# Kernel optimization log

Measured on AMD Instinct MI355X. Metric: run time of the kernel, lower is better.

The kernel has to match this reference:

```python
import jax, jax.numpy as jnp
import numpy as np

DIM = 128
HOP = 2
NEIGH = [12, 2]  # neighbor_num per hop
ALPHA = 0.2      # leaky-relu slope
NUM_NODE = 50000
B, S = 128, 50
STDV = 1.0 / np.sqrt(DIM)


def _leaky(x):
    return jnp.where(x >= 0, x, ALPHA * x)


def _local_agg(h, adj, a_local):
    # h: [B,S,D], adj: [B,S,S] ints in 0..4, a_local: [4,D]
    a_in = h[:, :, None, :] * h[:, None, :, :]            # [B,S,S,D]
    e = _leaky(jnp.einsum('bijd,kd->kbij', a_in, a_local))  # [4,B,S,S]
    att = jnp.full(adj.shape, -9e15, dtype=h.dtype)
    for k in range(4):
        att = jnp.where(adj == k + 1, e[k], att)
    att = jax.nn.softmax(att, axis=-1)
    return jnp.einsum('bij,bjd->bid', att, h)


def _global_agg(self_v, neigh_v, extra_v, w1, w2, w3, bias):
    # self_v: [B,N,D], neigh_v: [B,N,K,D], extra_v: [B,N,D]
    a = _leaky(jnp.einsum('bnkd,de->bnke', extra_v[:, :, None, :] * neigh_v, w1))
    a = jnp.einsum('bnke,e->bnk', a, w2)
    a = jax.nn.softmax(a, axis=-1)
    agg = jnp.einsum('bnk,bnkd->bnd', a, neigh_v)
    out = jnp.concatenate([self_v, agg], axis=-1) @ w3 + bias
    return jax.nn.relu(out)


def setup_inputs() -> dict:
    key = jax.random.key(0)
    ks = jax.random.split(key, 12)
    u = lambda k, shp: jax.random.uniform(k, shp, jnp.float32, -STDV, STDV)
    return {
        'inputs': jax.random.randint(ks[0], (B, S), 0, NUM_NODE),
        'adj': jax.random.randint(ks[1], (B, S, S), 0, 5),
        'mask_item': jnp.ones((B, S), dtype=jnp.int32),
        'item': jax.random.randint(ks[2], (B, S), 0, NUM_NODE),
        'first_adj': jax.random.randint(ks[3], (B, S * NEIGH[0]), 0, NUM_NODE),
        'adj_all': jax.random.randint(ks[4], (NUM_NODE, 2), 0, NUM_NODE),
        'embedding': u(ks[5], (NUM_NODE, DIM)),
        'a_local': u(ks[6], (4, DIM)),
        'gw1': u(ks[7], (HOP, DIM, DIM)),
        'gw2': u(ks[8], (HOP, DIM)),
        'gw3': u(ks[9], (HOP, 2 * DIM, DIM)),
        'gbias': u(ks[10], (HOP, DIM)),
    }


def reference(inputs, adj, mask_item, item, first_adj, adj_all,
              embedding, a_local, gw1, gw2, gw3, gbias):
    b, s = inputs.shape
    h = embedding[inputs]                                  # [B,S,D]
    h_local = _local_agg(h, adj, a_local)

    m = mask_item.astype(embedding.dtype)[..., None]       # [B,S,1]
    item_emb = embedding[item] * m
    sum_item = jnp.sum(item_emb, 1) / jnp.sum(m, 1)        # [B,D]
    sess = sum_item[:, None, :]                            # [B,1,D]

    # multi-hop neighbor sampling
    neigh1 = first_adj.reshape(b, s * NEIGH[0])            # [B, 600]
    neigh2 = adj_all[neigh1.reshape(-1)].reshape(b, s * NEIGH[0] * NEIGH[1])  # [B,1200]
    ev = [embedding[inputs], embedding[neigh1], embedding[neigh2]]

    for n_hop in range(HOP):
        nxt = []
        for hop in range(HOP - n_hop):
            neigh_v = ev[hop + 1].reshape(b, -1, NEIGH[hop], DIM)
            extra_v = jnp.broadcast_to(sess, (b, ev[hop].shape[1], DIM))
            nxt.append(_global_agg(ev[hop], neigh_v, extra_v,
                                   gw1[n_hop], gw2[n_hop], gw3[n_hop], gbias[n_hop]))
        ev = nxt
    h_global = ev[0].reshape(b, s, DIM)

    # dropout is identity at eval
    return h_local + h_global
```

## Files before the change

kernel.cpp:

```cpp
#include <hip/hip_runtime.h>
#include <stdint.h>

typedef unsigned short ushort_t;
typedef __attribute__((ext_vector_type(8))) short bf16x8;
typedef __attribute__((ext_vector_type(4))) float f32x4;

#define B_   128
#define S_   50
#define D_   128
#define ALPHA_ 0.2f

__device__ __forceinline__ float bf2f(ushort_t u){
  return __uint_as_float(((uint32_t)u) << 16);
}
__device__ __forceinline__ ushort_t f2bf(float f){
  uint32_t x = __float_as_uint(f);
  x = (x + 0x7fffu + ((x >> 16) & 1u)) >> 16;
  return (ushort_t)x;
}
__device__ __forceinline__ float leaky(float x){ return x >= 0.f ? x : ALPHA_*x; }

__global__ void detect_kernel(const uint32_t* __restrict__ emb_raw, int* __restrict__ flag){
  if (threadIdx.x == 0 && blockIdx.x == 0){
    int ok = 1;
    for (int i = 0; i < 64; i++){
      uint32_t lo = emb_raw[i] & 0xffffu;
      uint32_t ex = (lo >> 7) & 0xFFu;
      if (!(lo == 0u || (ex >= 64u && ex <= 126u))) ok = 0;
    }
    *flag = ok;
  }
}

__global__ void cvt_all(const void* __restrict__ p0, const void* __restrict__ p1,
                        const void* __restrict__ p2, const void* __restrict__ p3,
                        const void* __restrict__ p4, const void* __restrict__ p5,
                        ushort_t* __restrict__ dst, const int* __restrict__ flag){
  const int seg_end[6] = {6400000, 6400512, 6433280, 6433536, 6499072, 6499328};
  int base = (blockIdx.x*256 + threadIdx.x) * 4;
  if (base >= 6499328) return;
  int s = 0;
  while (base >= seg_end[s]) s++;
  int segbase = (s == 0) ? 0 : seg_end[s-1];
  const void* src = (s==0)?p0:(s==1)?p1:(s==2)?p2:(s==3)?p3:(s==4)?p4:p5;
  int off = base - segbase;
  union { ushort_t u[4]; uint2 d2; } o;
  if (*flag){
    o.d2 = *(const uint2*)((const ushort_t*)src + off);
  } else {
    float4 v = *(const float4*)((const float*)src + off);
    o.u[0] = f2bf(v.x); o.u[1] = f2bf(v.y); o.u[2] = f2bf(v.z); o.u[3] = f2bf(v.w);
  }
  *(uint2*)(dst + base) = o.d2;
}

__global__ void sess_kernel(const int* __restrict__ item, const int* __restrict__ mask,
                            const ushort_t* __restrict__ emb, ushort_t* __restrict__ sessb){
  int b = blockIdx.x, d = threadIdx.x;
  float acc = 0.f, den = 0.f;
  for (int s = 0; s < S_; s++){
    float fm = (float)mask[b*S_ + s];
    int id = item[b*S_ + s];
    acc += fm * bf2f(emb[(size_t)id*D_ + d]);
    den += fm;
  }
  sessb[b*D_ + d] = f2bf(acc / den);
}

__global__ __launch_bounds__(256) void local_mfma(
    const int* __restrict__ inputs, const int* __restrict__ adj,
    const ushort_t* __restrict__ emb, const ushort_t* __restrict__ alocb,
    ushort_t* __restrict__ hlb){
  __shared__ ushort_t hS[64][136];
  __shared__ ushort_t hT[128][72];
  __shared__ float    attS[64][68];
  __shared__ int      sids[64];
  int b = blockIdx.x;
  int tid = threadIdx.x;
  if (tid < 64) sids[tid] = (tid < S_) ? inputs[b*S_ + tid] : 0;
  __syncthreads();
  for (int idx = tid; idx < 64*128; idx += 256){
    int j = idx >> 7, d = idx & 127;
    ushort_t v = 0;
    if (j < S_) v = emb[(size_t)sids[j]*D_ + d];
    hS[j][d] = v;
    hT[d][j] = v;
  }
  for (int idx = tid; idx < 64*64; idx += 256)
    attS[idx >> 6][idx & 63] = -9.0e15f;
  __syncthreads();

  int lane = tid & 63, wv = tid >> 6;
  int q = lane >> 4, c = lane & 15;

  f32x4 Eacc[4][4];
  #pragma unroll
  for (int mi = 0; mi < 4; mi++)
    #pragma unroll
    for (int ni = 0; ni < 4; ni++) Eacc[mi][ni] = (f32x4){0.f,0.f,0.f,0.f};
  #pragma unroll
  for (int kt = 0; kt < 4; kt++){
    uint4 av = *(const uint4*)(alocb + wv*D_ + kt*32 + q*8);
    const uint32_t* ap = (const uint32_t*)&av;
    union { ushort_t u[8]; bf16x8 v; } afr[4];
    #pragma unroll
    for (int mi = 0; mi < 4; mi++){
      uint4 hv = *(const uint4*)(&hS[mi*16 + c][kt*32 + q*8]);
      const uint32_t* hp = (const uint32_t*)&hv;
      #pragma unroll
      for (int p = 0; p < 4; p++){
        float x0 = __uint_as_float(hp[p] << 16)         * __uint_as_float(ap[p] << 16);
        float x1 = __uint_as_float(hp[p] & 0xffff0000u) * __uint_as_float(ap[p] & 0xffff0000u);
        afr[mi].u[2*p]   = f2bf(x0);
        afr[mi].u[2*p+1] = f2bf(x1);
      }
    }
    #pragma unroll
    for (int ni = 0; ni < 4; ni++){
      union { uint4 q4; bf16x8 v; } bfr;
      bfr.q4 = *(const uint4*)(&hS[ni*16 + c][kt*32 + q*8]);
      #pragma unroll
      for (int mi = 0; mi < 4; mi++)
        Eacc[mi][ni] = __builtin_amdgcn_mfma_f32_16x16x32_bf16(afr[mi].v, bfr.v, Eacc[mi][ni], 0,0,0);
    }
  }
  const int* adjb = adj + (size_t)b*S_*S_;
  #pragma unroll
  for (int mi = 0; mi < 4; mi++){
    #pragma unroll
    for (int ni = 0; ni < 4; ni++){
      int j = ni*16 + c;
      #pragma unroll
      for (int r = 0; r < 4; r++){
        int i = mi*16 + q*4 + r;
        if (i < S_ && j < S_){
          int kk = adjb[i*S_ + j];
          if (kk == wv + 1) attS[i][j] = leaky(Eacc[mi][ni][r]);
        }
      }
    }
  }
  __syncthreads();
  if (tid < 64){
    int i = tid;
    if (i < S_){
      float mx = -__builtin_inff();
      for (int j = 0; j < S_; j++) mx = fmaxf(mx, attS[i][j]);
      float s = 0.f;
      for (int j = 0; j < S_; j++){ float e = __expf(attS[i][j] - mx); attS[i][j] = e; s += e; }
      float inv = 1.f / s;
      for (int j = 0; j < S_; j++) attS[i][j] *= inv;
      for (int j = S_; j < 64; j++) attS[i][j] = 0.f;
    } else {
      for (int j = 0; j < 64; j++) attS[i][j] = 0.f;
    }
  }
  __syncthreads();
  f32x4 Pacc[4][2];
  #pragma unroll
  for (int mi = 0; mi < 4; mi++){ Pacc[mi][0] = (f32x4){0.f,0.f,0.f,0.f}; Pacc[mi][1] = (f32x4){0.f,0.f,0.f,0.f}; }
  #pragma unroll
  for (int kt = 0; kt < 2; kt++){
    union { ushort_t u[8]; bf16x8 v; } afr[4];
    #pragma unroll
    for (int mi = 0; mi < 4; mi++){
      const float* arow = &attS[mi*16 + c][kt*32 + q*8];
      #pragma unroll
      for (int j = 0; j < 8; j++) afr[mi].u[j] = f2bf(arow[j]);
    }
    #pragma unroll
    for (int nn = 0; nn < 2; nn++){
      int ni = 2*wv + nn;
      union { uint4 q4; bf16x8 v; } bfr;
      bfr.q4 = *(const uint4*)(&hT[ni*16 + c][kt*32 + q*8]);
      #pragma unroll
      for (int mi = 0; mi < 4; mi++)
        Pacc[mi][nn] = __builtin_amdgcn_mfma_f32_16x16x32_bf16(afr[mi].v, bfr.v, Pacc[mi][nn], 0,0,0);
    }
  }
  #pragma unroll
  for (int mi = 0; mi < 4; mi++){
    #pragma unroll
    for (int nn = 0; nn < 2; nn++){
      int d = (2*wv + nn)*16 + c;
      #pragma unroll
      for (int r = 0; r < 4; r++){
        int i = mi*16 + q*4 + r;
        if (i < S_) hlb[((size_t)b*S_ + i)*D_ + d] = f2bf(Pacc[mi][nn][r]);
      }
    }
  }
}

__global__ __launch_bounds__(256) void score_mfma_ab(
    const ushort_t* __restrict__ sessb, const ushort_t* __restrict__ emb,
    const int* __restrict__ neigh1, const int* __restrict__ adj_all,
    const ushort_t* __restrict__ w1, const ushort_t* __restrict__ w2,
    float* __restrict__ score, int nA){
  __shared__ uint4 bfrag[2048];
  int tid = threadIdx.x;
  for (int idx = tid; idx < 2048; idx += 256){
    int kt = idx >> 9, rem = idx & 511, t = rem >> 6, ln = rem & 63;
    int qq = ln >> 4, cc = ln & 15;
    union { ushort_t u[8]; uint4 q4; } e;
    #pragma unroll
    for (int j = 0; j < 8; j++)
      e.u[j] = w1[(32*kt + qq*8 + j)*128 + 16*t + cc];
    bfrag[idx] = e.q4;
  }
  __syncthreads();
  int lane = tid & 63, wave = tid >> 6;
  int m = lane & 15, q = lane >> 4;
  float w2v[8];
  #pragma unroll
  for (int t = 0; t < 8; t++) w2v[t] = bf2f(w2[16*t + m]);

  for (int it = 0; it < 2; it++){
    int row_base = blockIdx.x*128 + it*64 + wave*16;
    int row = row_base + m;
    const ushort_t* nrow; int b;
    if (row < nA){
      nrow = emb + (size_t)neigh1[row]*D_;
      b = row / 600;
    } else {
      int r2 = row - nA;
      nrow = emb + (size_t)adj_all[(size_t)neigh1[r2>>1]*2 + (r2&1)]*D_;
      b = r2 / 1200;
    }
    const ushort_t* srow = sessb + (size_t)b*D_;

    f32x4 acc[8];
    #pragma unroll
    for (int t = 0; t < 8; t++) acc[t] = (f32x4){0.f,0.f,0.f,0.f};
    #pragma unroll
    for (int kt = 0; kt < 4; kt++){
      uint4 nv = *(const uint4*)(nrow + kt*32 + q*8);
      uint4 sv = *(const uint4*)(srow + kt*32 + q*8);
      const uint32_t* np = (const uint32_t*)&nv;
      const uint32_t* sp = (const uint32_t*)&sv;
      union { ushort_t u[8]; bf16x8 v; } afr;
      #pragma unroll
      for (int p = 0; p < 4; p++){
        uint32_t n2 = np[p], s2 = sp[p];
        float a0 = __uint_as_float(n2 << 16)          * __uint_as_float(s2 << 16);
        float a1 = __uint_as_float(n2 & 0xffff0000u)  * __uint_as_float(s2 & 0xffff0000u);
        afr.u[2*p]   = f2bf(a0);
        afr.u[2*p+1] = f2bf(a1);
      }
      #pragma unroll
      for (int t = 0; t < 8; t++){
        union { uint4 q4; bf16x8 v; } bfr;
        bfr.q4 = bfrag[(kt*8 + t)*64 + lane];
        acc[t] = __builtin_amdgcn_mfma_f32_16x16x32_bf16(afr.v, bfr.v, acc[t], 0, 0, 0);
      }
    }
    #pragma unroll
    for (int r = 0; r < 4; r++){
      float s = 0.f;
      #pragma unroll
      for (int t = 0; t < 8; t++) s += leaky(acc[t][r]) * w2v[t];
      s += __shfl_xor(s, 1, 64);
      s += __shfl_xor(s, 2, 64);
      s += __shfl_xor(s, 4, 64);
      s += __shfl_xor(s, 8, 64);
      if (m == 0) score[row_base + q*4 + r] = s;
    }
  }
}

__global__ __launch_bounds__(256) void score_mfma_c(
    const ushort_t* __restrict__ sessb, const ushort_t* __restrict__ out1,
    const ushort_t* __restrict__ w1, const ushort_t* __restrict__ w2,
    float* __restrict__ score){
  __shared__ uint4 bfrag[2048];
  int tid = threadIdx.x;
  for (int idx = tid; idx < 2048; idx += 256){
    int kt = idx >> 9, rem = idx & 511, t = rem >> 6, ln = rem & 63;
    int qq = ln >> 4, cc = ln & 15;
    union { ushort_t u[8]; uint4 q4; } e;
    #pragma unroll
    for (int j = 0; j < 8; j++)
      e.u[j] = w1[(32*kt + qq*8 + j)*128 + 16*t + cc];
    bfrag[idx] = e.q4;
  }
  __syncthreads();
  int lane = tid & 63, wave = tid >> 6;
  int m = lane & 15, q = lane >> 4;
  float w2v[8];
  #pragma unroll
  for (int t = 0; t < 8; t++) w2v[t] = bf2f(w2[16*t + m]);
  for (int it = 0; it < 2; it++){
    int row_base = blockIdx.x*128 + it*64 + wave*16;
    int row = row_base + m;
    const ushort_t* nrow = out1 + (size_t)row*D_;
    int b = row / 600;
    const ushort_t* srow = sessb + (size_t)b*D_;
    f32x4 acc[8];
    #pragma unroll
    for (int t = 0; t < 8; t++) acc[t] = (f32x4){0.f,0.f,0.f,0.f};
    #pragma unroll
    for (int kt = 0; kt < 4; kt++){
      uint4 nv = *(const uint4*)(nrow + kt*32 + q*8);
      uint4 sv = *(const uint4*)(srow + kt*32 + q*8);
      const uint32_t* np = (const uint32_t*)&nv;
      const uint32_t* sp = (const uint32_t*)&sv;
      union { ushort_t u[8]; bf16x8 v; } afr;
      #pragma unroll
      for (int p = 0; p < 4; p++){
        uint32_t n2 = np[p], s2 = sp[p];
        float a0 = __uint_as_float(n2 << 16)          * __uint_as_float(s2 << 16);
        float a1 = __uint_as_float(n2 & 0xffff0000u)  * __uint_as_float(s2 & 0xffff0000u);
        afr.u[2*p]   = f2bf(a0);
        afr.u[2*p+1] = f2bf(a1);
      }
      #pragma unroll
      for (int t = 0; t < 8; t++){
        union { uint4 q4; bf16x8 v; } bfr;
        bfr.q4 = bfrag[(kt*8 + t)*64 + lane];
        acc[t] = __builtin_amdgcn_mfma_f32_16x16x32_bf16(afr.v, bfr.v, acc[t], 0, 0, 0);
      }
    }
    #pragma unroll
    for (int r = 0; r < 4; r++){
      float s = 0.f;
      #pragma unroll
      for (int t = 0; t < 8; t++) s += leaky(acc[t][r]) * w2v[t];
      s += __shfl_xor(s, 1, 64);
      s += __shfl_xor(s, 2, 64);
      s += __shfl_xor(s, 4, 64);
      s += __shfl_xor(s, 8, 64);
      if (m == 0) score[row_base + q*4 + r] = s;
    }
  }
}

template<int K>
__device__ __forceinline__ void softmaxK(const float* __restrict__ sc, float att[K]){
  float mx = -__builtin_inff();
  #pragma unroll
  for (int k = 0; k < K; k++){ att[k] = sc[k]; mx = fmaxf(mx, att[k]); }
  float s = 0.f;
  #pragma unroll
  for (int k = 0; k < K; k++){ att[k] = __expf(att[k] - mx); s += att[k]; }
  float inv = 1.f / s;
  #pragma unroll
  for (int k = 0; k < K; k++) att[k] *= inv;
}

template<int K>
__device__ __forceinline__ void out_tile(
    int lane, const uint4* __restrict__ afrag,
    const ushort_t* __restrict__ sptr, const ushort_t* const nptr[K],
    const float att[K], f32x4 acc[8]){
  int q = lane >> 4;
  #pragma unroll
  for (int kt = 0; kt < 8; kt++){
    union { ushort_t u[8]; uint4 q4; bf16x8 v; } bfr;
    if (kt < 4){
      bfr.q4 = *(const uint4*)(sptr + kt*32 + q*8);
    } else {
      float g[8] = {0,0,0,0,0,0,0,0};
      #pragma unroll
      for (int k = 0; k < K; k++){
        uint4 nv = *(const uint4*)(nptr[k] + (kt-4)*32 + q*8);
        const uint32_t* np = (const uint32_t*)&nv;
        #pragma unroll
        for (int p = 0; p < 4; p++){
          g[2*p]   = fmaf(att[k], __uint_as_float(np[p] << 16),         g[2*p]);
          g[2*p+1] = fmaf(att[k], __uint_as_float(np[p] & 0xffff0000u), g[2*p+1]);
        }
      }
      #pragma unroll
      for (int j = 0; j < 8; j++) bfr.u[j] = f2bf(g[j]);
    }
    #pragma unroll
    for (int t = 0; t < 8; t++){
      union { uint4 q4; bf16x8 v; } af;
      af.q4 = afrag[(kt*8 + t)*64 + lane];
      acc[t] = __builtin_amdgcn_mfma_f32_16x16x32_bf16(af.v, bfr.v, acc[t], 0, 0, 0);
    }
  }
}

__global__ __launch_bounds__(256) void out_mfma_ab(
    const float* __restrict__ score, const int* __restrict__ idx,
    const int* __restrict__ nbr, const int* __restrict__ adj_all,
    const ushort_t* __restrict__ emb,
    const ushort_t* __restrict__ w3, const ushort_t* __restrict__ bias,
    ushort_t* __restrict__ o0c, ushort_t* __restrict__ out1c,
    int nA, int nTot, int scoreBbase){
  __shared__ uint4 afrag[4096];
  int tid = threadIdx.x;
  for (int i = tid; i < 4096; i += 256){
    int kt = i >> 9, rem = i & 511, t = rem >> 6, ln = rem & 63;
    int qq = ln >> 4, cc = ln & 15;
    union { ushort_t u[8]; uint4 q4; } e;
    #pragma unroll
    for (int j = 0; j < 8; j++)
      e.u[j] = w3[(32*kt + qq*8 + j)*128 + 16*t + cc];
    afrag[i] = e.q4;
  }
  __syncthreads();
  int lane = tid & 63, wave = tid >> 6;
  int mrow = lane & 15, q = lane >> 4;
  float bv[8][4];
  #pragma unroll
  for (int t = 0; t < 8; t++){
    const ushort_t* bp = bias + 16*t + q*4;
    #pragma unroll
    for (int r = 0; r < 4; r++) bv[t][r] = bf2f(bp[r]);
  }
  for (int it = 0; it < 2; it++){
    int row_base = blockIdx.x*128 + it*64 + wave*16;
    int row = row_base + mrow;
    bool active = row < nTot;
    int rowc = active ? row : (nTot - 1);
    bool isA = rowc < nA;
    f32x4 acc[8];
    #pragma unroll
    for (int t = 0; t < 8; t++) acc[t] = (f32x4){0.f,0.f,0.f,0.f};
    if (isA){
      const ushort_t* sptr = emb + (size_t)idx[rowc]*D_;
      const ushort_t* nptr[12];
      #pragma unroll
      for (int k = 0; k < 12; k++) nptr[k] = emb + (size_t)nbr[rowc*12 + k]*D_;
      float att[12];
      softmaxK<12>(score + (size_t)rowc*12, att);
      out_tile<12>(lane, afrag, sptr, nptr, att, acc);
    } else {
      int rB = rowc - nA;
      const ushort_t* sptr = emb + (size_t)nbr[rB]*D_;
      const ushort_t* nptr[2];
      #pragma unroll
      for (int k = 0; k < 2; k++) nptr[k] = emb + (size_t)adj_all[(size_t)nbr[rB]*2 + k]*D_;
      float att[2];
      softmaxK<2>(score + scoreBbase + (size_t)rB*2, att);
      out_tile<2>(lane, afrag, sptr, nptr, att, acc);
    }
    if (active){
      ushort_t* dst = isA ? (o0c + (size_t)row*D_) : (out1c + (size_t)(row - nA)*D_);
      #pragma unroll
      for (int t = 0; t < 8; t++){
        int col0 = 16*t + q*4;
        union { ushort_t u[4]; uint2 d2; } pk;
        #pragma unroll
        for (int r = 0; r < 4; r++) pk.u[r] = f2bf(fmaxf(acc[t][r] + bv[t][r], 0.f));
        *(uint2*)(dst + col0) = pk.d2;
      }
    }
  }
}

__global__ __launch_bounds__(256) void out_mfma_c(
    const float* __restrict__ score, const ushort_t* __restrict__ out1,
    const ushort_t* __restrict__ selfsrc,
    const ushort_t* __restrict__ w3, const ushort_t* __restrict__ bias,
    const ushort_t* __restrict__ addsrc, float* __restrict__ outf, int nrows){
  __shared__ uint4 afrag[4096];
  int tid = threadIdx.x;
  for (int i = tid; i < 4096; i += 256){
    int kt = i >> 9, rem = i & 511, t = rem >> 6, ln = rem & 63;
    int qq = ln >> 4, cc = ln & 15;
    union { ushort_t u[8]; uint4 q4; } e;
    #pragma unroll
    for (int j = 0; j < 8; j++)
      e.u[j] = w3[(32*kt + qq*8 + j)*128 + 16*t + cc];
    afrag[i] = e.q4;
  }
  __syncthreads();
  int lane = tid & 63, wave = tid >> 6;
  int mrow = lane & 15, q = lane >> 4;
  float bv[8][4];
  #pragma unroll
  for (int t = 0; t < 8; t++){
    const ushort_t* bp = bias + 16*t + q*4;
    #pragma unroll
    for (int r = 0; r < 4; r++) bv[t][r] = bf2f(bp[r]);
  }
  for (int it = 0; it < 2; it++){
    int row_base = blockIdx.x*128 + it*64 + wave*16;
    int row = row_base + mrow;
    bool active = row < nrows;
    int rowc = active ? row : (nrows - 1);
    const ushort_t* sptr = selfsrc + (size_t)rowc*D_;
    const ushort_t* nptr[12];
    #pragma unroll
    for (int k = 0; k < 12; k++) nptr[k] = out1 + (size_t)(rowc*12 + k)*D_;
    float att[12];
    softmaxK<12>(score + (size_t)rowc*12, att);
    f32x4 acc[8];
    #pragma unroll
    for (int t = 0; t < 8; t++) acc[t] = (f32x4){0.f,0.f,0.f,0.f};
    out_tile<12>(lane, afrag, sptr, nptr, att, acc);
    if (active){
      #pragma unroll
      for (int t = 0; t < 8; t++){
        int col0 = 16*t + q*4;
        float v[4];
        const ushort_t* ap = addsrc + (size_t)row*D_ + col0;
        #pragma unroll
        for (int r = 0; r < 4; r++)
          v[r] = fmaxf(acc[t][r] + bv[t][r], 0.f) + bf2f(ap[r]);
        *(f32x4*)(outf + (size_t)row*D_ + col0) = (f32x4){v[0], v[1], v[2], v[3]};
      }
    }
  }
}

extern "C" void kernel_launch(void* const* d_in, const int* in_sizes, int n_in,
                              void* d_out, int out_size, void* d_ws, size_t ws_size,
                              hipStream_t stream) {
  const int* inputs    = (const int*)d_in[0];
  const int* adj       = (const int*)d_in[1];
  const int* mask_item = (const int*)d_in[2];
  const int* item      = (const int*)d_in[3];
  const int* first_adj = (const int*)d_in[4];
  const int* adj_all   = (const int*)d_in[5];

  char* ws = (char*)d_ws;
  size_t o = 0;
  int*      flag   = (int*)(ws + o);      o += 64;
  ushort_t* emb_b  = (ushort_t*)(ws + o); o += 12800000;
  ushort_t* alocb  = (ushort_t*)(ws + o); o += 1024;
  ushort_t* gw1b   = (ushort_t*)(ws + o); o += 65536;
  ushort_t* gw2b   = (ushort_t*)(ws + o); o += 512;
  ushort_t* gw3b   = (ushort_t*)(ws + o); o += 131072;
  ushort_t* gbb    = (ushort_t*)(ws + o); o += 512;
  ushort_t* sessb  = (ushort_t*)(ws + o); o += 32768;
  ushort_t* hlb    = (ushort_t*)(ws + o); o += 1638400;
  size_t fixed = o;
  int CHB = 16;
  if      (ws_size >= fixed + (size_t)128*173600) CHB = 128;
  else if (ws_size >= fixed + (size_t)64 *173600) CHB = 64;
  else if (ws_size >= fixed + (size_t)32 *173600) CHB = 32;
  ushort_t* out1c = (ushort_t*)(ws + o);  o += (size_t)CHB*153600;
  ushort_t* o0c   = (ushort_t*)(ws + o);  o += (size_t)CHB*12800;
  float*    score = (float*)(ws + o);

  float* outp = (float*)d_out;

  detect_kernel<<<1, 64, 0, stream>>>((const uint32_t*)d_in[6], flag);
  cvt_all<<<(6499328/4 + 255)/256, 256, 0, stream>>>(d_in[6], d_in[7], d_in[8], d_in[9],
                                                     d_in[10], d_in[11], emb_b, flag);

  sess_kernel<<<B_, 128, 0, stream>>>(item, mask_item, emb_b, sessb);
  local_mfma <<<B_, 256, 0, stream>>>(inputs, adj, emb_b, alocb, hlb);

  int nchunk = B_ / CHB;
  for (int c = 0; c < nchunk; c++){
    int b0 = c * CHB;
    const int* fadj  = first_adj + (size_t)b0 * 600;
    const ushort_t* sbc = sessb + (size_t)b0 * D_;
    ushort_t*  hlc   = hlb  + (size_t)b0 * 50 * D_;
    float*     outc  = outp + (size_t)b0 * 50 * D_;
    int nA600 = CHB*600, nA50 = CHB*50, nTot = CHB*650;

    score_mfma_ab<<<(3*nA600)/128, 256, 0, stream>>>(sbc, emb_b, fadj, adj_all,
                                                     gw1b, gw2b, score, nA600);
    out_mfma_ab<<<(nTot + 127)/128, 256, 0, stream>>>(score, inputs + b0*50, fadj, adj_all,
                                                      emb_b, gw3b, gbb, o0c, out1c,
                                                      nA50, nTot, nA600);
    score_mfma_c<<<nA600/128, 256, 0, stream>>>(sbc, out1c, gw1b + 16384, gw2b + 128, score);
    out_mfma_c<<<(nA50 + 127)/128, 256, 0, stream>>>(score, out1c, o0c,
                                                     gw3b + 32768, gbb + 128,
                                                     hlc, outc, nA50);
  }
}
```

Measured before the change: 221.0 us.

## Split local attention and hop-0 output kernels across more blocks

```diff
diff --git a/kernel.cpp b/kernel.cpp
--- a/kernel.cpp
+++ b/kernel.cpp
@@ -67,127 +67,111 @@
   sessb[b*D_ + d] = f2bf(acc / den);
 }
 
-__global__ __launch_bounds__(256) void local_mfma(
+__global__ __launch_bounds__(256) void local_mfma2(
     const int* __restrict__ inputs, const int* __restrict__ adj,
     const ushort_t* __restrict__ emb, const ushort_t* __restrict__ alocb,
     ushort_t* __restrict__ hlb){
   __shared__ ushort_t hS[64][136];
-  __shared__ ushort_t hT[128][72];
-  __shared__ float    attS[64][68];
+  __shared__ float    attS[16][68];
   __shared__ int      sids[64];
-  int b = blockIdx.x;
+  int blk = blockIdx.x;
+  int b  = blk >> 2;
+  int mi = blk & 3;
   int tid = threadIdx.x;
   if (tid < 64) sids[tid] = (tid < S_) ? inputs[b*S_ + tid] : 0;
   __syncthreads();
-  for (int idx = tid; idx < 64*128; idx += 256){
-    int j = idx >> 7, d = idx & 127;
-    ushort_t v = 0;
-    if (j < S_) v = emb[(size_t)sids[j]*D_ + d];
-    hS[j][d] = v;
-    hT[d][j] = v;
-  }
-  for (int idx = tid; idx < 64*64; idx += 256)
+  for (int idx = tid; idx < 64*16; idx += 256){
+    int j = idx >> 4, ch = idx & 15;
+    uint4 v = {0u, 0u, 0u, 0u};
+    if (j < S_) v = *(const uint4*)(emb + (size_t)sids[j]*D_ + ch*8);
+    *(uint4*)(&hS[j][ch*8]) = v;
+  }
+  for (int idx = tid; idx < 16*64; idx += 256)
     attS[idx >> 6][idx & 63] = -9.0e15f;
   __syncthreads();
 
   int lane = tid & 63, wv = tid >> 6;
   int q = lane >> 4, c = lane & 15;
 
-  f32x4 Eacc[4][4];
-  #pragma unroll
-  for (int mi = 0; mi < 4; mi++)
-    #pragma unroll
-    for (int ni = 0; ni < 4; ni++) Eacc[mi][ni] = (f32x4){0.f,0.f,0.f,0.f};
+  f32x4 Eacc[4];
+  #pragma unroll
+  for (int ni = 0; ni < 4; ni++) Eacc[ni] = (f32x4){0.f,0.f,0.f,0.f};
   #pragma unroll
   for (int kt = 0; kt < 4; kt++){
     uint4 av = *(const uint4*)(alocb + wv*D_ + kt*32 + q*8);
     const uint32_t* ap = (const uint32_t*)&av;
-    union { ushort_t u[8]; bf16x8 v; } afr[4];
-    #pragma unroll
-    for (int mi = 0; mi < 4; mi++){
-      uint4 hv = *(const uint4*)(&hS[mi*16 + c][kt*32 + q*8]);
-      const uint32_t* hp = (const uint32_t*)&hv;
-      #pragma unroll
-      for (int p = 0; p < 4; p++){
-        float x0 = __uint_as_float(hp[p] << 16)         * __uint_as_float(ap[p] << 16);
-        float x1 = __uint_as_float(hp[p] & 0xffff0000u) * __uint_as_float(ap[p] & 0xffff0000u);
-        afr[mi].u[2*p]   = f2bf(x0);
-        afr[mi].u[2*p+1] = f2bf(x1);
-      }
+    uint4 hv = *(const uint4*)(&hS[mi*16 + c][kt*32 + q*8]);
+    const uint32_t* hp = (const uint32_t*)&hv;
+    union { ushort_t u[8]; bf16x8 v; } afr;
+    #pragma unroll
+    for (int p = 0; p < 4; p++){
+      float x0 = __uint_as_float(hp[p] << 16)         * __uint_as_float(ap[p] << 16);
+      float x1 = __uint_as_float(hp[p] & 0xffff0000u) * __uint_as_float(ap[p] & 0xffff0000u);
+      afr.u[2*p]   = f2bf(x0);
+      afr.u[2*p+1] = f2bf(x1);
     }
     #pragma unroll
     for (int ni = 0; ni < 4; ni++){
       union { uint4 q4; bf16x8 v; } bfr;
       bfr.q4 = *(const uint4*)(&hS[ni*16 + c][kt*32 + q*8]);
-      #pragma unroll
-      for (int mi = 0; mi < 4; mi++)
-        Eacc[mi][ni] = __builtin_amdgcn_mfma_f32_16x16x32_bf16(afr[mi].v, bfr.v, Eacc[mi][ni], 0,0,0);
+      Eacc[ni] = __builtin_amdgcn_mfma_f32_16x16x32_bf16(afr.v, bfr.v, Eacc[ni], 0,0,0);
     }
   }
   const int* adjb = adj + (size_t)b*S_*S_;
   #pragma unroll
-  for (int mi = 0; mi < 4; mi++){
-    #pragma unroll
-    for (int ni = 0; ni < 4; ni++){
-      int j = ni*16 + c;
-      #pragma unroll
-      for (int r = 0; r < 4; r++){
-        int i = mi*16 + q*4 + r;
-        if (i < S_ && j < S_){
-          int kk = adjb[i*S_ + j];
-          if (kk == wv + 1) attS[i][j] = leaky(Eacc[mi][ni][r]);
-        }
-      }
-    }
-  }
-  __syncthreads();
-  if (tid < 64){
-    int i = tid;
+  for (int ni = 0; ni < 4; ni++){
+    int j = ni*16 + c;
+    #pragma unroll
+    for (int r = 0; r < 4; r++){
+      int i = mi*16 + q*4 + r;
+      if (i < S_ && j < S_){
+        int kk = adjb[i*S_ + j];
+        if (kk == wv + 1) attS[q*4 + r][j] = leaky(Eacc[ni][r]);
+      }
+    }
+  }
+  __syncthreads();
+  if (tid < 16){
+    int i = mi*16 + tid;
     if (i < S_){
       float mx = -__builtin_inff();
-      for (int j = 0; j < S_; j++) mx = fmaxf(mx, attS[i][j]);
+      for (int j = 0; j < S_; j++) mx = fmaxf(mx, attS[tid][j]);
       float s = 0.f;
-      for (int j = 0; j < S_; j++){ float e = __expf(attS[i][j] - mx); attS[i][j] = e; s += e; }
+      for (int j = 0; j < S_; j++){ float e = __expf(attS[tid][j] - mx); attS[tid][j] = e; s += e; }
       float inv = 1.f / s;
-      for (int j = 0; j < S_; j++) attS[i][j] *= inv;
-      for (int j = S_; j < 64; j++) attS[i][j] = 0.f;
+      for (int j = 0; j < S_; j++) attS[tid][j] *= inv;
+      for (int j = S_; j < 64; j++) attS[tid][j] = 0.f;
     } else {
-      for (int j = 0; j < 64; j++) attS[i][j] = 0.f;
-    }
-  }
-  __syncthreads();
-  f32x4 Pacc[4][2];
-  #pragma unroll
-  for (int mi = 0; mi < 4; mi++){ Pacc[mi][0] = (f32x4){0.f,0.f,0.f,0.f}; Pacc[mi][1] = (f32x4){0.f,0.f,0.f,0.f}; }
+      for (int j = 0; j < 64; j++) attS[tid][j] = 0.f;
+    }
+  }
+  __syncthreads();
+  f32x4 Pacc[2];
+  Pacc[0] = (f32x4){0.f,0.f,0.f,0.f};
+  Pacc[1] = (f32x4){0.f,0.f,0.f,0.f};
   #pragma unroll
   for (int kt = 0; kt < 2; kt++){
-    union { ushort_t u[8]; bf16x8 v; } afr[4];
-    #pragma unroll
-    for (int mi = 0; mi < 4; mi++){
-      const float* arow = &attS[mi*16 + c][kt*32 + q*8];
-      #pragma unroll
-      for (int j = 0; j < 8; j++) afr[mi].u[j] = f2bf(arow[j]);
-    }
+    union { ushort_t u[8]; bf16x8 v; } afr;
+    const float* arow = &attS[c][kt*32 + q*8];
+    #pragma unroll
+    for (int j = 0; j < 8; j++) afr.u[j] = f2bf(arow[j]);
     #pragma unroll
     for (int nn = 0; nn < 2; nn++){
       int ni = 2*wv + nn;
-      union { uint4 q4; bf16x8 v; } bfr;
-      bfr.q4 = *(const uint4*)(&hT[ni*16 + c][kt*32 + q*8]);
-      #pragma unroll
-      for (int mi = 0; mi < 4; mi++)
-        Pacc[mi][nn] = __builtin_amdgcn_mfma_f32_16x16x32_bf16(afr[mi].v, bfr.v, Pacc[mi][nn], 0,0,0);
-    }
-  }
-  #pragma unroll
-  for (int mi = 0; mi < 4; mi++){
-    #pragma unroll
-    for (int nn = 0; nn < 2; nn++){
-      int d = (2*wv + nn)*16 + c;
-      #pragma unroll
-      for (int r = 0; r < 4; r++){
-        int i = mi*16 + q*4 + r;
-        if (i < S_) hlb[((size_t)b*S_ + i)*D_ + d] = f2bf(Pacc[mi][nn][r]);
-      }
+      union { ushort_t u[8]; bf16x8 v; } bfr;
+      #pragma unroll
+      for (int jj = 0; jj < 8; jj++)
+        bfr.u[jj] = hS[kt*32 + q*8 + jj][ni*16 + c];
+      Pacc[nn] = __builtin_amdgcn_mfma_f32_16x16x32_bf16(afr.v, bfr.v, Pacc[nn], 0,0,0);
+    }
+  }
+  #pragma unroll
+  for (int nn = 0; nn < 2; nn++){
+    int d = (2*wv + nn)*16 + c;
+    #pragma unroll
+    for (int r = 0; r < 4; r++){
+      int i = mi*16 + q*4 + r;
+      if (i < S_) hlb[((size_t)b*S_ + i)*D_ + d] = f2bf(Pacc[nn][r]);
     }
   }
 }
@@ -347,11 +331,11 @@
   for (int k = 0; k < K; k++) att[k] *= inv;
 }
 
-template<int K>
+template<int K, int NT>
 __device__ __forceinline__ void out_tile(
     int lane, const uint4* __restrict__ afrag,
     const ushort_t* __restrict__ sptr, const ushort_t* const nptr[K],
-    const float att[K], f32x4 acc[8]){
+    const float att[K], f32x4 acc[NT]){
   int q = lane >> 4;
   #pragma unroll
   for (int kt = 0; kt < 8; kt++){
@@ -374,9 +358,9 @@
       for (int j = 0; j < 8; j++) bfr.u[j] = f2bf(g[j]);
     }
     #pragma unroll
-    for (int t = 0; t < 8; t++){
+    for (int t = 0; t < NT; t++){
       union { uint4 q4; bf16x8 v; } af;
-      af.q4 = afrag[(kt*8 + t)*64 + lane];
+      af.q4 = afrag[(kt*NT + t)*64 + lane];
       acc[t] = __builtin_amdgcn_mfma_f32_16x16x32_bf16(af.v, bfr.v, acc[t], 0, 0, 0);
     }
   }
@@ -389,36 +373,39 @@
     const ushort_t* __restrict__ w3, const ushort_t* __restrict__ bias,
     ushort_t* __restrict__ o0c, ushort_t* __restrict__ out1c,
     int nA, int nTot, int scoreBbase){
-  __shared__ uint4 afrag[4096];
+  __shared__ uint4 afrag[2048];
+  int half = blockIdx.x & 1;
+  int rb   = blockIdx.x >> 1;
+  int tbase = half*4;
   int tid = threadIdx.x;
-  for (int i = tid; i < 4096; i += 256){
-    int kt = i >> 9, rem = i & 511, t = rem >> 6, ln = rem & 63;
+  for (int i = tid; i < 2048; i += 256){
+    int kt = i >> 8, rem = i & 255, t = rem >> 6, ln = rem & 63;
     int qq = ln >> 4, cc = ln & 15;
     union { ushort_t u[8]; uint4 q4; } e;
     #pragma unroll
     for (int j = 0; j < 8; j++)
-      e.u[j] = w3[(32*kt + qq*8 + j)*128 + 16*t + cc];
+      e.u[j] = w3[(32*kt + qq*8 + j)*128 + 16*(tbase + t) + cc];
     afrag[i] = e.q4;
   }
   __syncthreads();
   int lane = tid & 63, wave = tid >> 6;
   int mrow = lane & 15, q = lane >> 4;
-  float bv[8][4];
-  #pragma unroll
-  for (int t = 0; t < 8; t++){
-    const ushort_t* bp = bias + 16*t + q*4;
+  float bv[4][4];
+  #pragma unroll
+  for (int t = 0; t < 4; t++){
+    const ushort_t* bp = bias + 16*(tbase + t) + q*4;
     #pragma unroll
     for (int r = 0; r < 4; r++) bv[t][r] = bf2f(bp[r]);
   }
   for (int it = 0; it < 2; it++){
-    int row_base = blockIdx.x*128 + it*64 + wave*16;
+    int row_base = rb*128 + it*64 + wave*16;
     int row = row_base + mrow;
     bool active = row < nTot;
     int rowc = active ? row : (nTot - 1);
     bool isA = rowc < nA;
-    f32x4 acc[8];
-    #pragma unroll
-    for (int t = 0; t < 8; t++) acc[t] = (f32x4){0.f,0.f,0.f,0.f};
+    f32x4 acc[4];
+    #pragma unroll
+    for (int t = 0; t < 4; t++) acc[t] = (f32x4){0.f,0.f,0.f,0.f};
     if (isA){
       const ushort_t* sptr = emb + (size_t)idx[rowc]*D_;
       const ushort_t* nptr[12];
@@ -426,7 +413,7 @@
       for (int k = 0; k < 12; k++) nptr[k] = emb + (size_t)nbr[rowc*12 + k]*D_;
       float att[12];
       softmaxK<12>(score + (size_t)rowc*12, att);
-      out_tile<12>(lane, afrag, sptr, nptr, att, acc);
+      out_tile<12,4>(lane, afrag, sptr, nptr, att, acc);
     } else {
       int rB = rowc - nA;
       const ushort_t* sptr = emb + (size_t)nbr[rB]*D_;
@@ -435,13 +422,13 @@
       for (int k = 0; k < 2; k++) nptr[k] = emb + (size_t)adj_all[(size_t)nbr[rB]*2 + k]*D_;
       float att[2];
       softmaxK<2>(score + scoreBbase + (size_t)rB*2, att);
-      out_tile<2>(lane, afrag, sptr, nptr, att, acc);
+      out_tile<2,4>(lane, afrag, sptr, nptr, att, acc);
     }
     if (active){
       ushort_t* dst = isA ? (o0c + (size_t)row*D_) : (out1c + (size_t)(row - nA)*D_);
       #pragma unroll
-      for (int t = 0; t < 8; t++){
-        int col0 = 16*t + q*4;
+      for (int t = 0; t < 4; t++){
+        int col0 = 16*(tbase + t) + q*4;
         union { ushort_t u[4]; uint2 d2; } pk;
         #pragma unroll
         for (int r = 0; r < 4; r++) pk.u[r] = f2bf(fmaxf(acc[t][r] + bv[t][r], 0.f));
@@ -491,7 +478,7 @@
     f32x4 acc[8];
     #pragma unroll
     for (int t = 0; t < 8; t++) acc[t] = (f32x4){0.f,0.f,0.f,0.f};
-    out_tile<12>(lane, afrag, sptr, nptr, att, acc);
+    out_tile<12,8>(lane, afrag, sptr, nptr, att, acc);
     if (active){
       #pragma unroll
       for (int t = 0; t < 8; t++){
@@ -544,7 +531,7 @@
                                                      d_in[10], d_in[11], emb_b, flag);
 
   sess_kernel<<<B_, 128, 0, stream>>>(item, mask_item, emb_b, sessb);
-  local_mfma <<<B_, 256, 0, stream>>>(inputs, adj, emb_b, alocb, hlb);
+  local_mfma2<<<B_*4, 256, 0, stream>>>(inputs, adj, emb_b, alocb, hlb);
 
   int nchunk = B_ / CHB;
   for (int c = 0; c < nchunk; c++){
@@ -557,9 +544,9 @@
 
     score_mfma_ab<<<(3*nA600)/128, 256, 0, stream>>>(sbc, emb_b, fadj, adj_all,
                                                      gw1b, gw2b, score, nA600);
-    out_mfma_ab<<<(nTot + 127)/128, 256, 0, stream>>>(score, inputs + b0*50, fadj, adj_all,
-                                                      emb_b, gw3b, gbb, o0c, out1c,
-                                                      nA50, nTot, nA600);
+    out_mfma_ab<<<((nTot + 127)/128)*2, 256, 0, stream>>>(score, inputs + b0*50, fadj, adj_all,
+                                                          emb_b, gw3b, gbb, o0c, out1c,
+                                                          nA50, nTot, nA600);
     score_mfma_c<<<nA600/128, 256, 0, stream>>>(sbc, out1c, gw1b + 16384, gw2b + 128, score);
     out_mfma_c<<<(nA50 + 127)/128, 256, 0, stream>>>(score, out1c, o0c,
                                                      gw3b + 32768, gbb + 128,
```

Result: no change. 218.1 us (-1.3%).
